# Optimization experiments

Hardware: AMD Instinct MI355X
Metric: run time of the kernel (lower is better)

Reference implementation:

```python
import jax, jax.numpy as jnp
import numpy as np

D_MODEL = 1024
N_HEADS = 16
HEAD_DIM = D_MODEL // N_HEADS
MAX_LEN = 2048
MAX_REL = MAX_LEN - 1  # max relative distance


def setup_inputs() -> dict:
    key = jax.random.key(0)
    ks = jax.random.split(key, 12)
    B, T, S = 2, 2048, 2048
    s = 1.0 / np.sqrt(D_MODEL)
    inp = {
        "query": jax.random.normal(ks[0], (B, T, D_MODEL), jnp.float32),
        "key": jax.random.normal(ks[1], (B, S, D_MODEL), jnp.float32),
        "value": jax.random.normal(ks[2], (B, S, D_MODEL), jnp.float32),
        "attn_mask": jnp.ones((B, 1, T, S), dtype=bool),
        "Wq": jax.random.normal(ks[3], (D_MODEL, D_MODEL), jnp.float32) * s,
        "bq": jnp.zeros((D_MODEL,), jnp.float32),
        "Wk": jax.random.normal(ks[4], (D_MODEL, D_MODEL), jnp.float32) * s,
        "bk": jnp.zeros((D_MODEL,), jnp.float32),
        "Wv": jax.random.normal(ks[5], (D_MODEL, D_MODEL), jnp.float32) * s,
        "bv": jnp.zeros((D_MODEL,), jnp.float32),
        "Wo": jax.random.normal(ks[6], (D_MODEL, D_MODEL), jnp.float32) * s,
        "bo": jnp.zeros((D_MODEL,), jnp.float32),
        "rel_emb": jax.random.normal(ks[7], (2 * MAX_REL + 1, N_HEADS), jnp.float32) * 0.02,
    }
    return inp


def _relative_bias(rel_emb, tgt_len, src_len):
    rel_pos = jnp.arange(tgt_len)[:, None] - jnp.arange(src_len)[None, :]
    rel_pos = jnp.clip(rel_pos, -MAX_REL, MAX_REL) + MAX_REL  # [T, S] indices
    bias = rel_emb[rel_pos]                 # [T, S, H]
    return jnp.transpose(bias, (2, 0, 1))[None]  # [1, H, T, S]


def reference(query, key, value, attn_mask, Wq, bq, Wk, bk, Wv, bv, Wo, bo, rel_emb):
    B, T, _ = query.shape
    S = key.shape[1]
    scale = HEAD_DIM ** -0.5
    # projections -> [B, H, L, Dh]
    q = (query @ Wq.T + bq).reshape(B, T, N_HEADS, HEAD_DIM).transpose(0, 2, 1, 3)
    k = (key @ Wk.T + bk).reshape(B, S, N_HEADS, HEAD_DIM).transpose(0, 2, 1, 3)
    v = (value @ Wv.T + bv).reshape(B, S, N_HEADS, HEAD_DIM).transpose(0, 2, 1, 3)
    scores = jnp.einsum("bhtd,bhsd->bhts", q, k) * scale
    scores = scores + _relative_bias(rel_emb, T, S)
    scores = jnp.where(attn_mask, scores, -jnp.inf)
    weights = jax.nn.softmax(scores, axis=-1)
    out = jnp.einsum("bhts,bhsd->bhtd", weights, v)
    out = out.transpose(0, 2, 1, 3).reshape(B, T, D_MODEL)
    return out @ Wo.T + bo
```

## Files before the change

### kernel.cpp

```cpp
#include <hip/hip_runtime.h>
#include <stdint.h>

#define TSEQ   2048
#define BATCH  2
#define DM     1024
#define NH     16
#define DH     64

typedef __attribute__((ext_vector_type(8))) short short8;
typedef __attribute__((ext_vector_type(4))) short short4v;
typedef __attribute__((ext_vector_type(4))) float f32x4;
typedef __attribute__((ext_vector_type(16))) float f32x16;
typedef unsigned short bfu;

__device__ __forceinline__ unsigned short f2bf(float f) {
  union { float f; unsigned int u; } x; x.f = f;
  unsigned int u = x.u + 0x7fffu + ((x.u >> 16) & 1u);
  return (unsigned short)(u >> 16);
}
__device__ __forceinline__ float bf2f(unsigned short s) {
  union { unsigned int u; float f; } x; x.u = ((unsigned int)s) << 16;
  return x.f;
}
__device__ __forceinline__ float u2f(unsigned int u) {
  union { unsigned int u; float f; } x; x.u = u;
  return x.f;
}
__device__ __forceinline__ float max3f(float a, float b, float c) {
  return fmaxf(fmaxf(a, b), c);
}

__device__ __forceinline__ void async16(const void* g, void* lds) {
  __builtin_amdgcn_global_load_lds(
      (const __attribute__((address_space(1))) void*)g,
      (__attribute__((address_space(3))) void*)lds, 16, 0, 0);
}

__device__ __forceinline__ f32x4 mfma16x16x32(short8 a, short8 b, f32x4 c) {
  return __builtin_amdgcn_mfma_f32_16x16x32_bf16(a, b, c, 0, 0, 0);
}
__device__ __forceinline__ f32x16 mfma32(short8 a, short8 b, f32x16 c) {
  return __builtin_amdgcn_mfma_f32_32x32x16_bf16(a, b, c, 0, 0, 0);
}
__device__ __forceinline__ unsigned int cvtpk(float lo, float hi) {
  unsigned int r;
  asm("v_cvt_pk_bf16_f32 %0, %1, %2" : "=v"(r) : "v"(lo), "v"(hi));
  return r;
}

struct CvtArgs { const float* src[7]; bfu* dst[7]; int n[7]; };

__global__ __launch_bounds__(256) void cvt_kernel(CvtArgs a) {
  const int t = blockIdx.y;
  const float* __restrict__ s = a.src[t];
  bfu* __restrict__ d = a.dst[t];
  const int n = a.n[t];
  for (int i = (blockIdx.x * 256 + threadIdx.x) * 4; i < n; i += gridDim.x * 256 * 4) {
    const float4 v = *(const float4*)(s + i);
    short4v o;
    o[0] = (short)f2bf(v.x); o[1] = (short)f2bf(v.y);
    o[2] = (short)f2bf(v.z); o[3] = (short)f2bf(v.w);
    *(short4v*)(d + i) = o;
  }
}

struct Gemm3 { const bfu* A[3]; const bfu* W[3]; const float* bias[3]; bfu* C[3]; };

__global__ __launch_bounds__(256) void gemm_qkv_kernel(Gemm3 g) {
  __shared__ bfu As[128 * 32];
  __shared__ bfu Bs[128 * 32];
  const int z = blockIdx.z;
  const bfu* __restrict__ A = g.A[z];
  const bfu* __restrict__ W = g.W[z];
  const float* __restrict__ bias = g.bias[z];
  bfu* __restrict__ C = g.C[z];

  const int tid = threadIdx.x;
  const int w = tid >> 6, lane = tid & 63;
  const int wr = w >> 1, wc = w & 1;
  const int m0 = blockIdx.x * 128, n0 = blockIdx.y * 128;

  f32x4 acc[4][4];
#pragma unroll
  for (int i = 0; i < 4; ++i)
#pragma unroll
    for (int j = 0; j < 4; ++j) acc[i][j] = (f32x4){0.f, 0.f, 0.f, 0.f};

  const int srow = lane >> 2;
  const int scol = (lane & 3) * 8;
  const int koff = (lane >> 4) * 8;
  const int frow = lane & 15;

  for (int kk = 0; kk < DM; kk += 32) {
#pragma unroll
    for (int j = 0; j < 2; ++j) {
      const int seg = w * 2 + j;
      const int r = seg * 16 + srow;
      async16(A + (size_t)(m0 + r) * DM + kk + scol, As + seg * 512);
      async16(W + (size_t)(n0 + r) * DM + kk + scol, Bs + seg * 512);
    }
    __syncthreads();
    short8 af[4], bfv[4];
#pragma unroll
    for (int m = 0; m < 4; ++m)
      af[m] = *(const short8*)(As + (wr * 64 + m * 16 + frow) * 32 + koff);
#pragma unroll
    for (int n = 0; n < 4; ++n)
      bfv[n] = *(const short8*)(Bs + (wc * 64 + n * 16 + frow) * 32 + koff);
#pragma unroll
    for (int m = 0; m < 4; ++m)
#pragma unroll
      for (int n = 0; n < 4; ++n)
        acc[m][n] = mfma16x16x32(af[m], bfv[n], acc[m][n]);
    __syncthreads();
  }

#pragma unroll
  for (int n = 0; n < 4; ++n) {
    const int col = n0 + wc * 64 + n * 16 + frow;
    const float bv = bias[col];
#pragma unroll
    for (int m = 0; m < 4; ++m) {
      const int rbase = m0 + wr * 64 + m * 16 + (lane >> 4) * 4;
#pragma unroll
      for (int r = 0; r < 4; ++r)
        C[(size_t)(rbase + r) * DM + col] = f2bf(acc[m][n][r] + bv);
    }
  }
}

__global__ __launch_bounds__(256) void gemm_o_kernel(const bfu* __restrict__ A, const bfu* __restrict__ W,
                                                     const float* __restrict__ bias, float* __restrict__ C) {
  __shared__ bfu As[128 * 32];
  __shared__ bfu Bs[64 * 32];
  const int tid = threadIdx.x;
  const int w = tid >> 6, lane = tid & 63;
  const int m0 = blockIdx.x * 128, n0 = blockIdx.y * 64;

  f32x4 acc[2][4];
#pragma unroll
  for (int i = 0; i < 2; ++i)
#pragma unroll
    for (int j = 0; j < 4; ++j) acc[i][j] = (f32x4){0.f, 0.f, 0.f, 0.f};

  const int srow = lane >> 2;
  const int scol = (lane & 3) * 8;
  const int koff = (lane >> 4) * 8;
  const int frow = lane & 15;

  for (int kk = 0; kk < DM; kk += 32) {
#pragma unroll
    for (int j = 0; j < 2; ++j) {
      const int seg = w * 2 + j;
      const int r = seg * 16 + srow;
      async16(A + (size_t)(m0 + r) * DM + kk + scol, As + seg * 512);
    }
    async16(W + (size_t)(n0 + w * 16 + srow) * DM + kk + scol, Bs + w * 512);
    __syncthreads();
    short8 af[2], bfv[4];
#pragma unroll
    for (int m = 0; m < 2; ++m)
      af[m] = *(const short8*)(As + (w * 32 + m * 16 + frow) * 32 + koff);
#pragma unroll
    for (int n = 0; n < 4; ++n)
      bfv[n] = *(const short8*)(Bs + (n * 16 + frow) * 32 + koff);
#pragma unroll
    for (int m = 0; m < 2; ++m)
#pragma unroll
      for (int n = 0; n < 4; ++n)
        acc[m][n] = mfma16x16x32(af[m], bfv[n], acc[m][n]);
    __syncthreads();
  }

#pragma unroll
  for (int n = 0; n < 4; ++n) {
    const int col = n0 + n * 16 + frow;
    const float bv = bias[col];
#pragma unroll
    for (int m = 0; m < 2; ++m) {
      const int rbase = m0 + w * 32 + m * 16 + (lane >> 4) * 4;
#pragma unroll
      for (int r = 0; r < 4; ++r)
        C[(size_t)(rbase + r) * DM + col] = acc[m][n][r] + bv;
    }
  }
}

__global__ __launch_bounds__(256) void vt_kernel(const bfu* __restrict__ V, bfu* __restrict__ Vt) {
  __shared__ bfu t[64][72];
  const int tid = threadIdx.x;
  const int b = blockIdx.z, hh = blockIdx.y, s0 = blockIdx.x * 64;
  const int r = tid >> 2, c0 = (tid & 3) * 16;
  const short8* src = (const short8*)(V + ((size_t)(b * TSEQ) + s0 + r) * DM + hh * DH + c0);
  const short8 v0 = src[0], v1 = src[1];
#pragma unroll
  for (int e = 0; e < 8; ++e) {
    t[c0 + e][r] = (bfu)v0[e];
    t[c0 + 8 + e][r] = (bfu)v1[e];
  }
  __syncthreads();
  const int d = tid >> 2, sc = (tid & 3) * 16;
  bfu* dst = Vt + ((size_t)(b * NH + hh) * DH + d) * TSEQ + s0 + sc;
  *(short8*)dst = *(const short8*)&t[d][sc];
  *(short8*)(dst + 8) = *(const short8*)&t[d][sc + 8];
}

union PF { unsigned int u[4]; short8 s8; };

__global__ __launch_bounds__(512, 4) void attn_kernel(const bfu* __restrict__ Qp, const bfu* __restrict__ Kp,
                                                      const bfu* __restrict__ VtG, const float* __restrict__ rel,
                                                      bfu* __restrict__ Op) {
  __shared__ __align__(16) char lds_raw[74304];
  unsigned int* wA = (unsigned int*)(lds_raw + 65536);
  unsigned int* wB = (unsigned int*)(lds_raw + 65536 + 4416);
  float* olds = (float*)lds_raw;
  float* mlds = (float*)(lds_raw + 33280);
  float* llds = (float*)(lds_raw + 33792);
  bfu*   ot   = (bfu*)(lds_raw + 34304);

  const int tid = threadIdx.x;
  const int wg = tid >> 6;
  const int w = wg & 3;
  const int sg = wg >> 2;
  const int lane = tid & 63;
  const int h = lane >> 5, l31 = lane & 31;
  const int b = blockIdx.z, hh = blockIdx.y;
  const int t0 = blockIdx.x * 128;
  const float L2E = 1.4426950408889634f;

  const size_t kbase0 = (size_t)(b * TSEQ) * DM + hh * DH;
  const size_t vbase0 = (size_t)(b * NH + hh) * DH * TSEQ;

  const int qrow = t0 + w * 32 + l31;
  short8 qb[4];
#pragma unroll
  for (int kk = 0; kk < 4; ++kk) {
    short8 v = *(const short8*)(Qp + (size_t)(b * TSEQ + qrow) * DM + hh * DH + kk * 16 + h * 8);
#pragma unroll
    for (int j = 0; j < 8; ++j) v[j] = (short)f2bf(bf2f((unsigned short)v[j]) * 0.125f);
    qb[kk] = v;
  }

  for (int k = tid; k < 1088; k += 512) {
    const int i0 = t0 + 2 * k;
    const int c0i = i0 > 4094 ? 4094 : i0;
    const int c1i = i0 + 1 > 4094 ? 4094 : i0 + 1;
    const int c2i = i0 + 2 > 4094 ? 4094 : i0 + 2;
    const unsigned int b0 = f2bf(rel[(size_t)c0i * NH + hh]);
    const unsigned int b1 = f2bf(rel[(size_t)c1i * NH + hh]);
    const unsigned int b2 = f2bf(rel[(size_t)c2i * NH + hh]);
    wA[k] = (b1 << 16) | b0;
    wB[k] = (b2 << 16) | b1;
  }

  int koff[2][4];
#pragma unroll
  for (int s = 0; s < 2; ++s)
#pragma unroll
    for (int kk = 0; kk < 4; ++kk)
      koff[s][kk] = (s * 32 + l31) * 64 + 8 * ((2 * kk + h) ^ (l31 & 7));

  const int bbase = w * 32 + l31 + 2047 - 4 * h;
  const int M0 = (bbase - 1) >> 1;
  const unsigned int* const bsel = ((bbase - 1) & 1) ? wB : wA;
  const unsigned int* qb0 = bsel + (M0 - sg * 512);

  const int r8 = lane >> 3, cc = lane & 7;
  char* const grpbase = lds_raw + sg * 32768;

  const int swz = 8 * (cc ^ r8);
  const bfu* kg0 = Kp + kbase0 + (size_t)(sg * 1024 + 8 * w + r8) * DM + swz;
  const bfu* kg1 = kg0 + (size_t)32 * DM;
  const bfu* vg0 = VtG + vbase0 + (size_t)(8 * w + r8) * TSEQ + sg * 1024 + swz;
  const bfu* vg1 = vg0 + (size_t)32 * TSEQ;

  auto stage = [&](int par) {
    bfu* Kb = (bfu*)(grpbase + par * 16384);
    bfu* Vb = (bfu*)(grpbase + par * 16384 + 8192);
    async16(kg0, Kb + w * 512);
    async16(kg1, Kb + (4 + w) * 512);
    async16(vg0, Vb + w * 512);
    async16(vg1, Vb + (4 + w) * 512);
    kg0 += (size_t)64 * DM; kg1 += (size_t)64 * DM;
    vg0 += 64; vg1 += 64;
  };

  f32x16 o0, o1;
#pragma unroll
  for (int i = 0; i < 16; ++i) { o0[i] = 0.f; o1[i] = 0.f; }
  float mrun = -1e30f, lrun = 0.f;

  stage(0);
  __syncthreads();

#pragma unroll 1
  for (int t = 0; t < 16; ++t) {
    if (t + 1 < 16) stage((t + 1) & 1);
    const bfu* Kb = (const bfu*)(grpbase + (t & 1) * 16384);
    const bfu* Vb = (const bfu*)(grpbase + (t & 1) * 16384 + 8192);

    f32x16 a0, a1;
#pragma unroll
    for (int pr = 0; pr < 8; ++pr) {
      const int e2 = (pr >> 1) * 4 + (pr & 1);
      const unsigned int u0 = qb0[-e2];
      const unsigned int u1 = qb0[-16 - e2];
      a0[2 * pr]     = u2f(u0 & 0xffff0000u);
      a0[2 * pr + 1] = u2f(u0 << 16);
      a1[2 * pr]     = u2f(u1 & 0xffff0000u);
      a1[2 * pr + 1] = u2f(u1 << 16);
    }
    qb0 -= 32;

    __builtin_amdgcn_s_setprio(1);
#pragma unroll
    for (int kk = 0; kk < 4; ++kk) {
      a0 = mfma32(*(const short8*)(Kb + koff[0][kk]), qb[kk], a0);
      a1 = mfma32(*(const short8*)(Kb + koff[1][kk]), qb[kk], a1);
    }
    __builtin_amdgcn_s_setprio(0);

    float x0 = max3f(a0[0], a0[1], a0[2]);
    float x1 = max3f(a0[3], a0[4], a0[5]);
    float x2 = max3f(a0[6], a0[7], a0[8]);
    float x3 = max3f(a0[9], a0[10], a0[11]);
    float x4 = max3f(a0[12], a0[13], a0[14]);
    float x5 = max3f(a0[15], a1[0], a1[1]);
    float x6 = max3f(a1[2], a1[3], a1[4]);
    float x7 = max3f(a1[5], a1[6], a1[7]);
    float x8 = max3f(a1[8], a1[9], a1[10]);
    float x9 = max3f(a1[11], a1[12], a1[13]);
    float x10 = fmaxf(a1[14], a1[15]);
    float mx = fmaxf(max3f(max3f(x0, x1, x2), max3f(x3, x4, x5), max3f(x6, x7, x8)),
                     fmaxf(x9, x10));
    mx = fmaxf(mx, __shfl_xor(mx, 32));

    if (mx > mrun + 8.f) {
      const float scl = __builtin_amdgcn_exp2f((mrun - mx) * L2E);
      mrun = mx;
      lrun *= scl;
#pragma unroll
      for (int i = 0; i < 16; ++i) { o0[i] *= scl; o1[i] *= scl; }
    }
    const float mf = mrun * L2E;
#pragma unroll
    for (int i = 0; i < 16; ++i) {
      a0[i] = __builtin_amdgcn_exp2f(a0[i] * L2E - mf);
      a1[i] = __builtin_amdgcn_exp2f(a1[i] * L2E - mf);
    }
    float t16[16];
#pragma unroll
    for (int i = 0; i < 16; ++i) t16[i] = a0[i] + a1[i];
#pragma unroll
    for (int i = 0; i < 8; ++i) t16[i] += t16[i + 8];
#pragma unroll
    for (int i = 0; i < 4; ++i) t16[i] += t16[i + 4];
    lrun += (t16[0] + t16[1]) + (t16[2] + t16[3]);

    __builtin_amdgcn_s_setprio(1);
#pragma unroll
    for (int ks = 0; ks < 4; ++ks) {
      const int o8 = (ks & 1) * 8;
      const f32x16& src = (ks < 2) ? a0 : a1;
      unsigned int pk0 = cvtpk(src[o8 + 0], src[o8 + 1]);
      unsigned int pk1 = cvtpk(src[o8 + 2], src[o8 + 3]);
      unsigned int pk2 = cvtpk(src[o8 + 4], src[o8 + 5]);
      unsigned int pk3 = cvtpk(src[o8 + 6], src[o8 + 7]);
      asm volatile("v_permlane32_swap_b32 %0, %1" : "+v"(pk0), "+v"(pk2));
      asm volatile("v_permlane32_swap_b32 %0, %1" : "+v"(pk1), "+v"(pk3));
      PF pf;
      pf.u[0] = pk0; pf.u[1] = pk1; pf.u[2] = pk2; pf.u[3] = pk3;
      o0 = mfma32(*(const short8*)(Vb + koff[0][ks]), pf.s8, o0);
      o1 = mfma32(*(const short8*)(Vb + koff[1][ks]), pf.s8, o1);
    }
    __builtin_amdgcn_s_setprio(0);

    __syncthreads();
  }

  lrun += __shfl_xor(lrun, 32);

  if (sg == 1) {
#pragma unroll
    for (int rg = 0; rg < 16; ++rg) {
      const int dl = (rg & 3) + 8 * (rg >> 2) + 4 * h;
      olds[(w * 32 + l31) * 65 + dl]      = o0[rg];
      olds[(w * 32 + l31) * 65 + 32 + dl] = o1[rg];
    }
    if (h == 0) { mlds[w * 32 + l31] = mrun; llds[w * 32 + l31] = lrun; }
  }
  __syncthreads();
  if (sg == 0) {
    const float m1 = mlds[w * 32 + l31];
    const float l1 = llds[w * 32 + l31];
    const float M = fmaxf(mrun, m1);
    const float s_self = __builtin_amdgcn_exp2f((mrun - M) * L2E);
    const float s_oth  = __builtin_amdgcn_exp2f((m1 - M) * L2E);
    const float linv = 1.f / (lrun * s_self + l1 * s_oth);
    const float cs = s_self * linv, co = s_oth * linv;
    const int qq = w * 32 + l31;
#pragma unroll
    for (int rg = 0; rg < 16; ++rg) {
      const int dl = (rg & 3) + 8 * (rg >> 2) + 4 * h;
      const float f0 = o0[rg] * cs + olds[qq * 65 + dl] * co;
      const float f1 = o1[rg] * cs + olds[qq * 65 + 32 + dl] * co;
      ot[qq * 72 + dl]      = f2bf(f0);
      ot[qq * 72 + 32 + dl] = f2bf(f1);
    }
  }
  __syncthreads();
  const int q2 = tid >> 2, seg = tid & 3;
  bfu* dst = Op + (size_t)(b * TSEQ + t0 + q2) * DM + hh * DH + seg * 16;
  *(short8*)dst       = *(const short8*)(ot + q2 * 72 + seg * 16);
  *(short8*)(dst + 8) = *(const short8*)(ot + q2 * 72 + seg * 16 + 8);
}

extern "C" void kernel_launch(void* const* d_in, const int* in_sizes, int n_in,
                              void* d_out, int out_size, void* d_ws, size_t ws_size,
                              hipStream_t stream) {
  (void)in_sizes; (void)n_in; (void)out_size; (void)ws_size;
  const float* query = (const float*)d_in[0];
  const float* key_  = (const float*)d_in[1];
  const float* value = (const float*)d_in[2];
  const float* Wq = (const float*)d_in[4];
  const float* bq = (const float*)d_in[5];
  const float* Wk = (const float*)d_in[6];
  const float* bk = (const float*)d_in[7];
  const float* Wv = (const float*)d_in[8];
  const float* bv = (const float*)d_in[9];
  const float* Wo = (const float*)d_in[10];
  const float* bo = (const float*)d_in[11];
  const float* rel = (const float*)d_in[12];
  float* out = (float*)d_out;

  const size_t SZ_X = (size_t)BATCH * TSEQ * DM;
  const size_t SZ_W = (size_t)DM * DM;

  char* p = (char*)d_ws;
  bfu* xq  = (bfu*)p; p += SZ_X * 2;
  bfu* xk  = (bfu*)p; p += SZ_X * 2;
  bfu* xv  = (bfu*)p; p += SZ_X * 2;
  bfu* wqb = (bfu*)p; p += SZ_W * 2;
  bfu* wkb = (bfu*)p; p += SZ_W * 2;
  bfu* wvb = (bfu*)p; p += SZ_W * 2;
  bfu* wob = (bfu*)p; p += SZ_W * 2;
  bfu* qp  = (bfu*)p; p += SZ_X * 2;
  bfu* kp  = (bfu*)p; p += SZ_X * 2;
  bfu* vt  = (bfu*)p; p += SZ_X * 2;
  bfu* ao  = (bfu*)p; p += SZ_X * 2;

  CvtArgs ca;
  ca.src[0] = query; ca.dst[0] = xq;  ca.n[0] = (int)SZ_X;
  ca.src[1] = key_;  ca.dst[1] = xk;  ca.n[1] = (int)SZ_X;
  ca.src[2] = value; ca.dst[2] = xv;  ca.n[2] = (int)SZ_X;
  ca.src[3] = Wq;    ca.dst[3] = wqb; ca.n[3] = (int)SZ_W;
  ca.src[4] = Wk;    ca.dst[4] = wkb; ca.n[4] = (int)SZ_W;
  ca.src[5] = Wv;    ca.dst[5] = wvb; ca.n[5] = (int)SZ_W;
  ca.src[6] = Wo;    ca.dst[6] = wob; ca.n[6] = (int)SZ_W;
  cvt_kernel<<<dim3(4096, 7), 256, 0, stream>>>(ca);

  Gemm3 g3;
  g3.A[0] = xq; g3.W[0] = wqb; g3.bias[0] = bq; g3.C[0] = qp;
  g3.A[1] = xk; g3.W[1] = wkb; g3.bias[1] = bk; g3.C[1] = kp;
  g3.A[2] = xv; g3.W[2] = wvb; g3.bias[2] = bv; g3.C[2] = ao;
  gemm_qkv_kernel<<<dim3(32, 8, 3), 256, 0, stream>>>(g3);

  vt_kernel<<<dim3(TSEQ / 64, NH, BATCH), 256, 0, stream>>>(ao, vt);

  attn_kernel<<<dim3(TSEQ / 128, NH, BATCH), 512, 0, stream>>>(qp, kp, vt, rel, ao);

  gemm_o_kernel<<<dim3(32, 16), 256, 0, stream>>>(ao, wob, bo, out);
}
```

Baseline: 128.8 us.

## Fuse fp32-to-bf16 activation conversion into QKV GEMM with double-buffered LDS

The QKV projection GEMM now reads the fp32 query/key/value activations directly, converts them to bf16 in registers and writes them into a swizzled LDS tile. The separate conversion pass over activations is removed, so the cvt kernel only converts weights. LDS is double-buffered, and the next tile's global loads are issued before the current MFMA work to overlap memory with compute. The cost is more register pressure from holding the fp32 A prefetch, and the A loads now move twice the bytes per element inside the GEMM.

```diff
diff --git a/kernel.cpp b/kernel.cpp
--- a/kernel.cpp
+++ b/kernel.cpp
@@ -11,6 +11,7 @@
 typedef __attribute__((ext_vector_type(4))) short short4v;
 typedef __attribute__((ext_vector_type(4))) float f32x4;
 typedef __attribute__((ext_vector_type(16))) float f32x16;
+typedef __attribute__((ext_vector_type(4))) unsigned int u32x4;
 typedef unsigned short bfu;
 
 __device__ __forceinline__ unsigned short f2bf(float f) {
@@ -48,7 +49,7 @@
   return r;
 }
 
-struct CvtArgs { const float* src[7]; bfu* dst[7]; int n[7]; };
+struct CvtArgs { const float* src[4]; bfu* dst[4]; int n[4]; };
 
 __global__ __launch_bounds__(256) void cvt_kernel(CvtArgs a) {
   const int t = blockIdx.y;
@@ -64,13 +65,13 @@
   }
 }
 
-struct Gemm3 { const bfu* A[3]; const bfu* W[3]; const float* bias[3]; bfu* C[3]; };
+struct Gemm3 { const float* A[3]; const bfu* W[3]; const float* bias[3]; bfu* C[3]; };
 
 __global__ __launch_bounds__(256) void gemm_qkv_kernel(Gemm3 g) {
-  __shared__ bfu As[128 * 32];
-  __shared__ bfu Bs[128 * 32];
+  __shared__ bfu As[2][128 * 32];
+  __shared__ bfu Bs[2][128 * 32];
   const int z = blockIdx.z;
-  const bfu* __restrict__ A = g.A[z];
+  const float* __restrict__ A = g.A[z];
   const bfu* __restrict__ W = g.W[z];
   const float* __restrict__ bias = g.bias[z];
   bfu* __restrict__ C = g.C[z];
@@ -88,30 +89,67 @@
 
   const int srow = lane >> 2;
   const int scol = (lane & 3) * 8;
-  const int koff = (lane >> 4) * 8;
   const int frow = lane & 15;
-
-  for (int kk = 0; kk < DM; kk += 32) {
+  const int q4 = lane >> 4;
+  const int koff = q4 * 8;
+  const int aro = 8 * (q4 ^ ((frow >> 1) & 3));
+
+  const int ar = tid >> 1;
+  const int ac = (tid & 1) * 16;
+  const int gsw = (ar >> 1) & 3;
+  const int d0 = (tid & 1) * 2;
+  const int apos0 = ar * 32 + 8 * (d0 ^ gsw);
+  const int apos1 = ar * 32 + 8 * ((d0 + 1) ^ gsw);
+  const float* const aptr = A + (size_t)(m0 + ar) * DM + ac;
+
+  float4 va0, va1, va2, va3;
+  auto loadA = [&](int kk) {
+    const float4* pa = (const float4*)(aptr + kk);
+    va0 = pa[0]; va1 = pa[1]; va2 = pa[2]; va3 = pa[3];
+  };
+  auto writeA = [&](int buf) {
+    u32x4 s0, s1;
+    s0[0] = cvtpk(va0.x, va0.y); s0[1] = cvtpk(va0.z, va0.w);
+    s0[2] = cvtpk(va1.x, va1.y); s0[3] = cvtpk(va1.z, va1.w);
+    s1[0] = cvtpk(va2.x, va2.y); s1[1] = cvtpk(va2.z, va2.w);
+    s1[2] = cvtpk(va3.x, va3.y); s1[3] = cvtpk(va3.z, va3.w);
+    *(u32x4*)(As[buf] + apos0) = s0;
+    *(u32x4*)(As[buf] + apos1) = s1;
+  };
+  auto stageW = [&](int kk, int buf) {
 #pragma unroll
     for (int j = 0; j < 2; ++j) {
       const int seg = w * 2 + j;
       const int r = seg * 16 + srow;
-      async16(A + (size_t)(m0 + r) * DM + kk + scol, As + seg * 512);
-      async16(W + (size_t)(n0 + r) * DM + kk + scol, Bs + seg * 512);
-    }
-    __syncthreads();
+      async16(W + (size_t)(n0 + r) * DM + kk + scol, Bs[buf] + seg * 512);
+    }
+  };
+
+  loadA(0);
+  stageW(0, 0);
+  writeA(0);
+  __syncthreads();
+
+#pragma unroll 1
+  for (int ks = 0; ks < 32; ++ks) {
+    const int cur = ks & 1;
+    if (ks + 1 < 32) {
+      loadA((ks + 1) * 32);
+      stageW((ks + 1) * 32, cur ^ 1);
+    }
     short8 af[4], bfv[4];
 #pragma unroll
     for (int m = 0; m < 4; ++m)
-      af[m] = *(const short8*)(As + (wr * 64 + m * 16 + frow) * 32 + koff);
+      af[m] = *(const short8*)(As[cur] + (wr * 64 + m * 16 + frow) * 32 + aro);
 #pragma unroll
     for (int n = 0; n < 4; ++n)
-      bfv[n] = *(const short8*)(Bs + (wc * 64 + n * 16 + frow) * 32 + koff);
+      bfv[n] = *(const short8*)(Bs[cur] + (wc * 64 + n * 16 + frow) * 32 + koff);
 #pragma unroll
     for (int m = 0; m < 4; ++m)
 #pragma unroll
       for (int n = 0; n < 4; ++n)
         acc[m][n] = mfma16x16x32(af[m], bfv[n], acc[m][n]);
+    if (ks + 1 < 32) writeA(cur ^ 1);
     __syncthreads();
   }
 
@@ -437,9 +475,7 @@
   const size_t SZ_W = (size_t)DM * DM;
 
   char* p = (char*)d_ws;
-  bfu* xq  = (bfu*)p; p += SZ_X * 2;
-  bfu* xk  = (bfu*)p; p += SZ_X * 2;
-  bfu* xv  = (bfu*)p; p += SZ_X * 2;
+  p += SZ_X * 2 * 3;
   bfu* wqb = (bfu*)p; p += SZ_W * 2;
   bfu* wkb = (bfu*)p; p += SZ_W * 2;
   bfu* wvb = (bfu*)p; p += SZ_W * 2;
@@ -450,19 +486,16 @@
   bfu* ao  = (bfu*)p; p += SZ_X * 2;
 
   CvtArgs ca;
-  ca.src[0] = query; ca.dst[0] = xq;  ca.n[0] = (int)SZ_X;
-  ca.src[1] = key_;  ca.dst[1] = xk;  ca.n[1] = (int)SZ_X;
-  ca.src[2] = value; ca.dst[2] = xv;  ca.n[2] = (int)SZ_X;
-  ca.src[3] = Wq;    ca.dst[3] = wqb; ca.n[3] = (int)SZ_W;
-  ca.src[4] = Wk;    ca.dst[4] = wkb; ca.n[4] = (int)SZ_W;
-  ca.src[5] = Wv;    ca.dst[5] = wvb; ca.n[5] = (int)SZ_W;
-  ca.src[6] = Wo;    ca.dst[6] = wob; ca.n[6] = (int)SZ_W;
-  cvt_kernel<<<dim3(4096, 7), 256, 0, stream>>>(ca);
+  ca.src[0] = Wq; ca.dst[0] = wqb; ca.n[0] = (int)SZ_W;
+  ca.src[1] = Wk; ca.dst[1] = wkb; ca.n[1] = (int)SZ_W;
+  ca.src[2] = Wv; ca.dst[2] = wvb; ca.n[2] = (int)SZ_W;
+  ca.src[3] = Wo; ca.dst[3] = wob; ca.n[3] = (int)SZ_W;
+  cvt_kernel<<<dim3(1024, 4), 256, 0, stream>>>(ca);
 
   Gemm3 g3;
-  g3.A[0] = xq; g3.W[0] = wqb; g3.bias[0] = bq; g3.C[0] = qp;
-  g3.A[1] = xk; g3.W[1] = wkb; g3.bias[1] = bk; g3.C[1] = kp;
-  g3.A[2] = xv; g3.W[2] = wvb; g3.bias[2] = bv; g3.C[2] = ao;
+  g3.A[0] = query; g3.W[0] = wqb; g3.bias[0] = bq; g3.C[0] = qp;
+  g3.A[1] = key_;  g3.W[1] = wkb; g3.bias[1] = bk; g3.C[1] = kp;
+  g3.A[2] = value; g3.W[2] = wvb; g3.bias[2] = bv; g3.C[2] = ao;
   gemm_qkv_kernel<<<dim3(32, 8, 3), 256, 0, stream>>>(g3);
 
   vt_kernel<<<dim3(TSEQ / 64, NH, BATCH), 256, 0, stream>>>(ao, vt);
```

Measured after the change: 134.7 us. 4.6% more time.

## Fuse fp32-to-bf16 activation conversion into QKV projection GEMM loads

Applied to the files above, without the earlier changes.

The QKV GEMM now loads the fp32 activations straight into LDS with a swizzled layout and converts them to bf16 in registers before the MFMA. The separate conversion pass over query/key/value is dropped, and the conversion kernel now handles only the weights. This removes a full read and write of three activation tensors. In exchange the GEMM reads twice as many activation bytes per tile and does extra conversion work inside its inner loop. Each A tile is still read by 8 column blocks.

```diff
diff --git a/kernel.cpp b/kernel.cpp
--- a/kernel.cpp
+++ b/kernel.cpp
@@ -48,7 +48,7 @@
   return r;
 }
 
-struct CvtArgs { const float* src[7]; bfu* dst[7]; int n[7]; };
+struct CvtArgs { const float* src[4]; bfu* dst[4]; int n[4]; };
 
 __global__ __launch_bounds__(256) void cvt_kernel(CvtArgs a) {
   const int t = blockIdx.y;
@@ -64,13 +64,13 @@
   }
 }
 
-struct Gemm3 { const bfu* A[3]; const bfu* W[3]; const float* bias[3]; bfu* C[3]; };
+struct Gemm3 { const float* A[3]; const bfu* W[3]; const float* bias[3]; bfu* C[3]; };
 
 __global__ __launch_bounds__(256) void gemm_qkv_kernel(Gemm3 g) {
-  __shared__ bfu As[128 * 32];
+  __shared__ float AsF[128 * 32];
   __shared__ bfu Bs[128 * 32];
   const int z = blockIdx.z;
-  const bfu* __restrict__ A = g.A[z];
+  const float* __restrict__ A = g.A[z];
   const bfu* __restrict__ W = g.W[z];
   const float* __restrict__ bias = g.bias[z];
   bfu* __restrict__ C = g.C[z];
@@ -88,22 +88,44 @@
 
   const int srow = lane >> 2;
   const int scol = (lane & 3) * 8;
-  const int koff = (lane >> 4) * 8;
   const int frow = lane & 15;
+  const int q4 = lane >> 4;
+  const int koff = q4 * 8;
+
+  int arow[4], acsw[4];
+#pragma unroll
+  for (int j = 0; j < 4; ++j) {
+    const int idx = j * 256 + tid;
+    arow[j] = idx >> 3;
+    acsw[j] = 4 * ((idx & 7) ^ (arow[j] & 7));
+  }
+  const int s0 = 4 * ((2 * q4) ^ (frow & 7));
+  const int s1 = 4 * ((2 * q4 + 1) ^ (frow & 7));
+
+  union U8 { unsigned int u[4]; short8 s8; };
 
   for (int kk = 0; kk < DM; kk += 32) {
+#pragma unroll
+    for (int j = 0; j < 4; ++j)
+      async16(A + (size_t)(m0 + arow[j]) * DM + kk + acsw[j], AsF + (j * 256 + w * 64) * 4);
 #pragma unroll
     for (int j = 0; j < 2; ++j) {
       const int seg = w * 2 + j;
       const int r = seg * 16 + srow;
-      async16(A + (size_t)(m0 + r) * DM + kk + scol, As + seg * 512);
       async16(W + (size_t)(n0 + r) * DM + kk + scol, Bs + seg * 512);
     }
     __syncthreads();
     short8 af[4], bfv[4];
 #pragma unroll
-    for (int m = 0; m < 4; ++m)
-      af[m] = *(const short8*)(As + (wr * 64 + m * 16 + frow) * 32 + koff);
+    for (int m = 0; m < 4; ++m) {
+      const int rb = (wr * 64 + m * 16 + frow) * 32;
+      const f32x4 u = *(const f32x4*)(AsF + rb + s0);
+      const f32x4 v = *(const f32x4*)(AsF + rb + s1);
+      U8 pk;
+      pk.u[0] = cvtpk(u[0], u[1]); pk.u[1] = cvtpk(u[2], u[3]);
+      pk.u[2] = cvtpk(v[0], v[1]); pk.u[3] = cvtpk(v[2], v[3]);
+      af[m] = pk.s8;
+    }
 #pragma unroll
     for (int n = 0; n < 4; ++n)
       bfv[n] = *(const short8*)(Bs + (wc * 64 + n * 16 + frow) * 32 + koff);
@@ -437,9 +459,7 @@
   const size_t SZ_W = (size_t)DM * DM;
 
   char* p = (char*)d_ws;
-  bfu* xq  = (bfu*)p; p += SZ_X * 2;
-  bfu* xk  = (bfu*)p; p += SZ_X * 2;
-  bfu* xv  = (bfu*)p; p += SZ_X * 2;
+  p += SZ_X * 2 * 3;
   bfu* wqb = (bfu*)p; p += SZ_W * 2;
   bfu* wkb = (bfu*)p; p += SZ_W * 2;
   bfu* wvb = (bfu*)p; p += SZ_W * 2;
@@ -450,19 +470,16 @@
   bfu* ao  = (bfu*)p; p += SZ_X * 2;
 
   CvtArgs ca;
-  ca.src[0] = query; ca.dst[0] = xq;  ca.n[0] = (int)SZ_X;
-  ca.src[1] = key_;  ca.dst[1] = xk;  ca.n[1] = (int)SZ_X;
-  ca.src[2] = value; ca.dst[2] = xv;  ca.n[2] = (int)SZ_X;
-  ca.src[3] = Wq;    ca.dst[3] = wqb; ca.n[3] = (int)SZ_W;
-  ca.src[4] = Wk;    ca.dst[4] = wkb; ca.n[4] = (int)SZ_W;
-  ca.src[5] = Wv;    ca.dst[5] = wvb; ca.n[5] = (int)SZ_W;
-  ca.src[6] = Wo;    ca.dst[6] = wob; ca.n[6] = (int)SZ_W;
-  cvt_kernel<<<dim3(4096, 7), 256, 0, stream>>>(ca);
+  ca.src[0] = Wq; ca.dst[0] = wqb; ca.n[0] = (int)SZ_W;
+  ca.src[1] = Wk; ca.dst[1] = wkb; ca.n[1] = (int)SZ_W;
+  ca.src[2] = Wv; ca.dst[2] = wvb; ca.n[2] = (int)SZ_W;
+  ca.src[3] = Wo; ca.dst[3] = wob; ca.n[3] = (int)SZ_W;
+  cvt_kernel<<<dim3(1024, 4), 256, 0, stream>>>(ca);
 
   Gemm3 g3;
-  g3.A[0] = xq; g3.W[0] = wqb; g3.bias[0] = bq; g3.C[0] = qp;
-  g3.A[1] = xk; g3.W[1] = wkb; g3.bias[1] = bk; g3.C[1] = kp;
-  g3.A[2] = xv; g3.W[2] = wvb; g3.bias[2] = bv; g3.C[2] = ao;
+  g3.A[0] = query; g3.W[0] = wqb; g3.bias[0] = bq; g3.C[0] = qp;
+  g3.A[1] = key_;  g3.W[1] = wkb; g3.bias[1] = bk; g3.C[1] = kp;
+  g3.A[2] = value; g3.W[2] = wvb; g3.bias[2] = bv; g3.C[2] = ao;
   gemm_qkv_kernel<<<dim3(32, 8, 3), 256, 0, stream>>>(g3);
 
   vt_kernel<<<dim3(TSEQ / 64, NH, BATCH), 256, 0, stream>>>(ao, vt);
```

New measurement: 123.5 us. 1.04x faster.
